# Performance work log

Hardware: AMD Instinct MI355X
Metric: run time of the kernel (lower is better)

## Reference

```python
import jax, jax.numpy as jnp
import numpy as np

N = 100000
E = 1600000
G = 64  # number of graphs
H = 128
BN_EPS = 1e-5


def setup_inputs() -> dict:
    key = jax.random.key(0)
    ks = jax.random.split(key, 12)
    x = jax.random.normal(ks[0], (N, 3), dtype=jnp.float32)
    edge_index = jax.random.randint(ks[1], (2, E), 0, N, dtype=jnp.int64)
    batch = jnp.sort(jax.random.randint(ks[2], (N,), 0, G, dtype=jnp.int64))
    W1 = jax.random.normal(ks[3], (3, H), dtype=jnp.float32) * 0.3
    W2 = jax.random.normal(ks[4], (H, H), dtype=jnp.float32) * 0.05
    W3 = jax.random.normal(ks[5], (H, H), dtype=jnp.float32) * 0.05
    lin_W = jax.random.normal(ks[6], (H, 2), dtype=jnp.float32) * 0.05
    d = {
        'x': x, 'edge_index': edge_index, 'batch': batch,
        'W1': W1, 'b1': jnp.zeros((H,), jnp.float32),
        'W2': W2, 'b2': jnp.zeros((H,), jnp.float32),
        'W3': W3, 'b3': jnp.zeros((H,), jnp.float32),
        'lin_W': lin_W, 'lin_b': jnp.zeros((2,), jnp.float32),
    }
    for i, kk in zip((1, 2, 3), ks[7:10]):
        d[f'bn{i}_g'] = jnp.ones((H,), jnp.float32)
        d[f'bn{i}_b'] = jnp.zeros((H,), jnp.float32)
        d[f'bn{i}_m'] = jnp.zeros((H,), jnp.float32)
        d[f'bn{i}_v'] = jax.random.uniform(kk, (H,), dtype=jnp.float32, minval=0.5, maxval=1.5)
    return d


def _gcn(x, src, dst, norm, W, b):
    # GCNConv: out = scatter_add(norm * (xW)[src], dst) + b
    h = x @ W
    msg = h[src] * norm[:, None]
    agg = jax.ops.segment_sum(msg, dst, num_segments=N)
    return agg + b


def _bn_eval(x, g, b, m, v):
    return (x - m) * jax.lax.rsqrt(v + BN_EPS) * g + b


def reference(x, edge_index, batch, W1, b1, W2, b2, W3, b3,
              bn1_g, bn1_b, bn1_m, bn1_v,
              bn2_g, bn2_b, bn2_m, bn2_v,
              bn3_g, bn3_b, bn3_m, bn3_v,
              lin_W, lin_b):
    loop = jnp.arange(N, dtype=edge_index.dtype)
    src = jnp.concatenate([edge_index[0], loop])
    dst = jnp.concatenate([edge_index[1], loop])
    # symmetric normalization with self-loops: deg from destination nodes
    deg = jax.ops.segment_sum(jnp.ones_like(dst, dtype=x.dtype), dst, num_segments=N)
    dinv = jnp.where(deg > 0, jax.lax.rsqrt(deg), 0.0)
    norm = dinv[src] * dinv[dst]

    h = jax.nn.relu(_bn_eval(_gcn(x, src, dst, norm, W1, b1), bn1_g, bn1_b, bn1_m, bn1_v))
    h = jax.nn.relu(_bn_eval(_gcn(h, src, dst, norm, W2, b2), bn2_g, bn2_b, bn2_m, bn2_v))
    h = jax.nn.relu(_bn_eval(_gcn(h, src, dst, norm, W3, b3), bn3_g, bn3_b, bn3_m, bn3_v))
    # dropout is identity in eval mode
    sums = jax.ops.segment_sum(h, batch, num_segments=G)
    cnts = jax.ops.segment_sum(jnp.ones((N,), h.dtype), batch, num_segments=G)
    pooled = sums / jnp.maximum(cnts, 1.0)[:, None]
    return pooled @ lin_W + lin_b
```

## Files before the change

kernel.cpp:

```cpp
#include <hip/hip_runtime.h>

#define NN 100000
#define EE 1600000
#define GG 64
#define HH 128
#define BN_EPS 1e-5f

#define CB 782
#define NB 256
#define TILE 6250

typedef unsigned short ushort_t;

static __device__ inline ushort_t f2bf(float f) {
    unsigned u = __float_as_uint(f);
    unsigned r = (u + 0x7FFF + ((u >> 16) & 1)) >> 16;
    return (ushort_t)r;
}
static __device__ inline float bf2f(ushort_t b) {
    return __uint_as_float(((unsigned)b) << 16);
}


__global__ __launch_bounds__(256) void k_hist(const int* __restrict__ ei,
                                              int* __restrict__ histG) {
    __shared__ int h[CB];
    int t = threadIdx.x;
    for (int i = t; i < CB; i += 256) h[i] = 0;
    __syncthreads();
    int e0 = blockIdx.x * TILE;
    for (int i = t; i < TILE; i += 256) {
        int d = ei[EE + e0 + i];
        atomicAdd(&h[d >> 7], 1);
    }
    __syncthreads();
    for (int i = t; i < CB; i += 256) histG[blockIdx.x * CB + i] = h[i];
}

__global__ __launch_bounds__(NB) void k_bscan(int* __restrict__ histG,
                                              int* __restrict__ total) {
    __shared__ int sh[NB];
    int t = threadIdx.x;
    int c = blockIdx.x;
    sh[t] = histG[t * CB + c];
    __syncthreads();
    for (int d = 1; d < NB; d <<= 1) {
        int x = (t >= d) ? sh[t - d] : 0;
        __syncthreads();
        sh[t] += x;
        __syncthreads();
    }
    histG[t * CB + c] = (t > 0) ? sh[t - 1] : 0;
    if (t == NB - 1) total[c] = sh[NB - 1];
}

__global__ __launch_bounds__(1024) void k_cbase(const int* __restrict__ total,
                                                int* __restrict__ cbase) {
    __shared__ int sh[1024];
    int t = threadIdx.x;
    sh[t] = (t < CB) ? total[t] : 0;
    __syncthreads();
    for (int d = 1; d < 1024; d <<= 1) {
        int x = (t >= d) ? sh[t - d] : 0;
        __syncthreads();
        sh[t] += x;
        __syncthreads();
    }
    if (t < CB) cbase[t] = (t > 0) ? sh[t - 1] : 0;
    if (t == CB - 1) cbase[CB] = sh[t];
}

__global__ __launch_bounds__(256) void k_cscatter(const int* __restrict__ ei,
                                                  const int* __restrict__ histG,
                                                  const int* __restrict__ cbase,
                                                  int* __restrict__ metaS) {
    __shared__ int base_l[CB];
    __shared__ int cur_l[CB];
    int t = threadIdx.x;
    int b = blockIdx.x;
    for (int i = t; i < CB; i += 256) {
        base_l[i] = cbase[i] + histG[b * CB + i];
        cur_l[i] = 0;
    }
    __syncthreads();
    int e0 = b * TILE;
    for (int i = t; i < TILE; i += 256) {
        int s = ei[e0 + i];
        int d = ei[EE + e0 + i];
        int c = d >> 7;
        int p = base_l[c] + atomicAdd(&cur_l[c], 1);
        metaS[p] = s | ((d & 127) << 17);
    }
}

__global__ __launch_bounds__(256) void k_fine(const int* __restrict__ metaS,
                                              const int* __restrict__ cbase,
                                              int* __restrict__ cnt,
                                              int* __restrict__ offs,
                                              int* __restrict__ col,
                                              float* __restrict__ dinv) {
    __shared__ int hist[128];
    __shared__ int scn[128];
    __shared__ int cur[128];
    int t = threadIdx.x;
    int c = blockIdx.x;
    int lo = cbase[c], hi = cbase[c + 1];
    if (t < 128) hist[t] = 0;
    __syncthreads();
    for (int r = lo + t; r < hi; r += 256) atomicAdd(&hist[metaS[r] >> 17], 1);
    __syncthreads();
    if (t < 128) scn[t] = hist[t];
    __syncthreads();
    for (int d = 1; d < 128; d <<= 1) {
        int x = (t >= d && t < 128) ? scn[t - d] : 0;
        __syncthreads();
        if (t < 128) scn[t] += x;
        __syncthreads();
    }
    if (t < 128) {
        int excl = (t > 0) ? scn[t - 1] : 0;
        cur[t] = excl;
        int node = c * 128 + t;
        if (node < NN) {
            cnt[node] = hist[t];
            offs[node] = lo + excl;
            dinv[node] = rsqrtf((float)(hist[t] + 1));
        }
    }
    __syncthreads();
    for (int r = lo + t; r < hi; r += 256) {
        int pk = metaS[r];
        int s = pk & 0x1FFFF;
        int idx = atomicAdd(&cur[pk >> 17], 1);
        col[lo + idx] = s;
    }
}


__global__ __launch_bounds__(256) void k_l12(const float* __restrict__ x,
                                             const int* __restrict__ offs,
                                             const int* __restrict__ cnt,
                                             const int* __restrict__ col,
                                             const float* __restrict__ dinv,
                                             const float* __restrict__ W1,
                                             const float* __restrict__ b1,
                                             const float* __restrict__ g1,
                                             const float* __restrict__ bb1,
                                             const float* __restrict__ m1,
                                             const float* __restrict__ v1,
                                             const float* __restrict__ W2,
                                             ushort_t* __restrict__ outB) {
    __shared__ float xs[64][132];
    __shared__ float4 ag[64];
    int tid = threadIdx.x;
    int row0 = blockIdx.x * 64;
    int hw = tid >> 5;
    int l = tid & 31;
    for (int k = 0; k < 8; k++) {
        int r = hw * 8 + k;
        int d = row0 + r;
        float a0 = 0.f, a1 = 0.f, a2 = 0.f;
        if (d < NN) {
            float dv = dinv[d];
            int base = offs[d], cn2 = cnt[d];
            for (int i = l; i < cn2; i += 32) {
                int s = col[base + i];
                float w = dinv[s] * dv;
                a0 += w * x[s * 3 + 0];
                a1 += w * x[s * 3 + 1];
                a2 += w * x[s * 3 + 2];
            }
#pragma unroll
            for (int off = 16; off >= 1; off >>= 1) {
                a0 += __shfl_xor(a0, off, 32);
                a1 += __shfl_xor(a1, off, 32);
                a2 += __shfl_xor(a2, off, 32);
            }
            if (l == 0) {
                float w0 = dv * dv;
                a0 += w0 * x[d * 3 + 0];
                a1 += w0 * x[d * 3 + 1];
                a2 += w0 * x[d * 3 + 2];
                ag[r] = make_float4(a0, a1, a2, 0.f);
            }
        } else if (l == 0) {
            ag[r] = make_float4(0.f, 0.f, 0.f, 0.f);
        }
    }
    __syncthreads();
    {
        int c = tid & 127;
        int rh = tid >> 7;
        float w0 = W1[c], w1 = W1[128 + c], w2 = W1[256 + c];
        float sc = g1[c] * rsqrtf(v1[c] + BN_EPS);
        float sh = (b1[c] - m1[c]) * sc + bb1[c];
#pragma unroll
        for (int i = 0; i < 32; i++) {
            int r = 2 * i + rh;
            float4 a = ag[r];
            float t = a.x * w0 + a.y * w1 + a.z * w2;
            xs[r][c] = fmaxf(t * sc + sh, 0.f);
        }
    }
    __syncthreads();
    int tx = tid & 31;
    int ty = tid >> 5;
    float acc[8][4];
#pragma unroll
    for (int i = 0; i < 8; i++)
#pragma unroll
        for (int j = 0; j < 4; j++) acc[i][j] = 0.f;
    const float* Wp = W2 + tx * 4;
#pragma unroll 4
    for (int k = 0; k < 128; k++) {
        float4 w = *(const float4*)&Wp[k * HH];
#pragma unroll
        for (int i = 0; i < 8; i++) {
            float xv = xs[ty * 8 + i][k];
            acc[i][0] += xv * w.x;
            acc[i][1] += xv * w.y;
            acc[i][2] += xv * w.z;
            acc[i][3] += xv * w.w;
        }
    }
    int c0 = tx * 4;
#pragma unroll
    for (int i = 0; i < 8; i++) {
        int gr = row0 + ty * 8 + i;
        if (gr < NN) {
            ushort4 o;
            o.x = f2bf(acc[i][0]);
            o.y = f2bf(acc[i][1]);
            o.z = f2bf(acc[i][2]);
            o.w = f2bf(acc[i][3]);
            size_t addr = (size_t)(c0 >> 6) * NN * 64 + (size_t)gr * 64 + (c0 & 63);
            *(ushort4*)&outB[addr] = o;
        }
    }
}


__global__ __launch_bounds__(256) void k_agg2(const ushort_t* __restrict__ t,
                                              const int* __restrict__ offs,
                                              const int* __restrict__ cnt,
                                              const int* __restrict__ col,
                                              const float* __restrict__ dinv,
                                              const float* __restrict__ bias,
                                              const float* __restrict__ g,
                                              const float* __restrict__ bb,
                                              const float* __restrict__ m,
                                              const float* __restrict__ v,
                                              ushort_t* __restrict__ out) {
    int slice = blockIdx.x & 1;
    int chunk = blockIdx.x >> 1;
    int tid = threadIdx.x;
    int lane = tid & 63;
    int wave = tid >> 6;
    int grp = lane >> 4;
    int l = lane & 15;
    int r = wave * 4 + grp;
    int d = chunk * 16 + r;
    int cl = l * 4;
    int c = slice * 64 + cl;
    const ushort_t* tS = t + (size_t)slice * NN * 64;
    float dvd = dinv[d];
    float w00 = dvd * dvd;
    ushort4 selfR = *(const ushort4*)&tS[(size_t)d * 64 + cl];
    float4 acc;
    acc.x = bf2f(selfR.x) * w00; acc.y = bf2f(selfR.y) * w00;
    acc.z = bf2f(selfR.z) * w00; acc.w = bf2f(selfR.w) * w00;
    int base = offs[d], cn2 = cnt[d];
    int lb = lane & ~15;
    for (int ib = 0; ib < cn2; ib += 16) {
        int i = ib + l;
        int s = 0;
        float w = 0.f;
        if (i < cn2) {
            s = col[base + i];
            w = dinv[s] * dvd;
        }
        int lim = min(16, cn2 - ib);
#pragma unroll 4
        for (int j = 0; j < lim; j++) {
            int ss = __shfl(s, lb + j);
            float ww = __shfl(w, lb + j);
            ushort4 tv = *(const ushort4*)&tS[(size_t)ss * 64 + cl];
            acc.x += ww * bf2f(tv.x);
            acc.y += ww * bf2f(tv.y);
            acc.z += ww * bf2f(tv.z);
            acc.w += ww * bf2f(tv.w);
        }
    }
    float4 gg = *(const float4*)&g[c];
    float4 vv = *(const float4*)&v[c];
    float4 mm = *(const float4*)&m[c];
    float4 bv = *(const float4*)&bb[c];
    float4 bi = *(const float4*)&bias[c];
    float sc0 = gg.x * rsqrtf(vv.x + BN_EPS);
    float sc1 = gg.y * rsqrtf(vv.y + BN_EPS);
    float sc2 = gg.z * rsqrtf(vv.z + BN_EPS);
    float sc3 = gg.w * rsqrtf(vv.w + BN_EPS);
    ushort4 o;
    o.x = f2bf(fmaxf(acc.x * sc0 + (bi.x - mm.x) * sc0 + bv.x, 0.f));
    o.y = f2bf(fmaxf(acc.y * sc1 + (bi.y - mm.y) * sc1 + bv.y, 0.f));
    o.z = f2bf(fmaxf(acc.z * sc2 + (bi.z - mm.z) * sc2 + bv.z, 0.f));
    o.w = f2bf(fmaxf(acc.w * sc3 + (bi.w - mm.w) * sc3 + bv.w, 0.f));
    *(ushort4*)&out[(size_t)slice * NN * 64 + (size_t)d * 64 + cl] = o;
}


__global__ __launch_bounds__(256) void k_mm(const ushort_t* __restrict__ xin,
                                            const float* __restrict__ W,
                                            ushort_t* __restrict__ outB) {
    __shared__ float xs[64][132];
    int tid = threadIdx.x;
    int tx = tid & 31;
    int ty = tid >> 5;
    int row0 = blockIdx.x * 64;
#pragma unroll
    for (int i = 0; i < 4; i++) {
        int idx8 = i * 256 + tid;
        int r = idx8 >> 4;
        int k8 = (idx8 & 15) * 8;
        int gr = row0 + r;
        size_t addr = (size_t)(k8 >> 6) * NN * 64 + (size_t)gr * 64 + (k8 & 63);
        int4 pk = (gr < NN) ? *(const int4*)&xin[addr] : make_int4(0, 0, 0, 0);
        float* dst = &xs[r][k8];
        dst[0] = __uint_as_float(((unsigned)pk.x) << 16);
        dst[1] = __uint_as_float(((unsigned)pk.x) & 0xFFFF0000u);
        dst[2] = __uint_as_float(((unsigned)pk.y) << 16);
        dst[3] = __uint_as_float(((unsigned)pk.y) & 0xFFFF0000u);
        dst[4] = __uint_as_float(((unsigned)pk.z) << 16);
        dst[5] = __uint_as_float(((unsigned)pk.z) & 0xFFFF0000u);
        dst[6] = __uint_as_float(((unsigned)pk.w) << 16);
        dst[7] = __uint_as_float(((unsigned)pk.w) & 0xFFFF0000u);
    }
    __syncthreads();
    float acc[8][4];
#pragma unroll
    for (int i = 0; i < 8; i++)
#pragma unroll
        for (int j = 0; j < 4; j++) acc[i][j] = 0.f;

    const float* Wp = W + tx * 4;
#pragma unroll 4
    for (int k = 0; k < 128; k++) {
        float4 w = *(const float4*)&Wp[k * HH];
#pragma unroll
        for (int i = 0; i < 8; i++) {
            float xv = xs[ty * 8 + i][k];
            acc[i][0] += xv * w.x;
            acc[i][1] += xv * w.y;
            acc[i][2] += xv * w.z;
            acc[i][3] += xv * w.w;
        }
    }
    int c0 = tx * 4;
#pragma unroll
    for (int i = 0; i < 8; i++) {
        int gr = row0 + ty * 8 + i;
        if (gr < NN) {
            ushort4 o;
            o.x = f2bf(acc[i][0]);
            o.y = f2bf(acc[i][1]);
            o.z = f2bf(acc[i][2]);
            o.w = f2bf(acc[i][3]);
            size_t addr = (size_t)(c0 >> 6) * NN * 64 + (size_t)gr * 64 + (c0 & 63);
            *(ushort4*)&outB[addr] = o;
        }
    }
}


__global__ __launch_bounds__(256) void k_aggpool2(const ushort_t* __restrict__ t,
                                                  const int* __restrict__ offs,
                                                  const int* __restrict__ cnt,
                                                  const int* __restrict__ col,
                                                  const float* __restrict__ dinv,
                                                  const float* __restrict__ bias,
                                                  const float* __restrict__ g,
                                                  const float* __restrict__ bb,
                                                  const float* __restrict__ m,
                                                  const float* __restrict__ v,
                                                  const int* __restrict__ batch,
                                                  float* __restrict__ gsum,
                                                  int* __restrict__ gcnt) {
    __shared__ float sh[16][64];
    __shared__ int bsh[16];
    int slice = blockIdx.x & 1;
    int chunk = blockIdx.x >> 1;
    int tid = threadIdx.x;
    int lane = tid & 63;
    int wave = tid >> 6;
    int grp = lane >> 4;
    int l = lane & 15;
    int r = wave * 4 + grp;
    int d = chunk * 16 + r;
    int cl = l * 4;
    int c = slice * 64 + cl;
    if (tid < 16) bsh[tid] = batch[chunk * 16 + tid];
    const ushort_t* tS = t + (size_t)slice * NN * 64;
    float dvd = dinv[d];
    float w00 = dvd * dvd;
    ushort4 selfR = *(const ushort4*)&tS[(size_t)d * 64 + cl];
    float4 acc;
    acc.x = bf2f(selfR.x) * w00; acc.y = bf2f(selfR.y) * w00;
    acc.z = bf2f(selfR.z) * w00; acc.w = bf2f(selfR.w) * w00;
    int base = offs[d], cn2 = cnt[d];
    int lb = lane & ~15;
    for (int ib = 0; ib < cn2; ib += 16) {
        int i = ib + l;
        int s = 0;
        float w = 0.f;
        if (i < cn2) {
            s = col[base + i];
            w = dinv[s] * dvd;
        }
        int lim = min(16, cn2 - ib);
#pragma unroll 4
        for (int j = 0; j < lim; j++) {
            int ss = __shfl(s, lb + j);
            float ww = __shfl(w, lb + j);
            ushort4 tv = *(const ushort4*)&tS[(size_t)ss * 64 + cl];
            acc.x += ww * bf2f(tv.x);
            acc.y += ww * bf2f(tv.y);
            acc.z += ww * bf2f(tv.z);
            acc.w += ww * bf2f(tv.w);
        }
    }
    float4 gg = *(const float4*)&g[c];
    float4 vv = *(const float4*)&v[c];
    float4 mm = *(const float4*)&m[c];
    float4 bv = *(const float4*)&bb[c];
    float4 bi = *(const float4*)&bias[c];
    float sc0 = gg.x * rsqrtf(vv.x + BN_EPS);
    float sc1 = gg.y * rsqrtf(vv.y + BN_EPS);
    float sc2 = gg.z * rsqrtf(vv.z + BN_EPS);
    float sc3 = gg.w * rsqrtf(vv.w + BN_EPS);
    float4 o;
    o.x = fmaxf(acc.x * sc0 + (bi.x - mm.x) * sc0 + bv.x, 0.f);
    o.y = fmaxf(acc.y * sc1 + (bi.y - mm.y) * sc1 + bv.y, 0.f);
    o.z = fmaxf(acc.z * sc2 + (bi.z - mm.z) * sc2 + bv.z, 0.f);
    o.w = fmaxf(acc.w * sc3 + (bi.w - mm.w) * sc3 + bv.w, 0.f);
    *(float4*)&sh[r][cl] = o;
    __syncthreads();
    if (tid < 64) {
        int cc = tid;
        float acc2 = 0.f;
        int cur = bsh[0];
        for (int rr = 0; rr < 16; rr++) {
            int g2 = bsh[rr];
            if (g2 != cur) {
                atomicAdd(&gsum[cur * HH + slice * 64 + cc], acc2);
                acc2 = 0.f; cur = g2;
            }
            acc2 += sh[rr][cc];
        }
        atomicAdd(&gsum[cur * HH + slice * 64 + cc], acc2);
    } else if (tid == 64 && slice == 0) {
        int cur = bsh[0];
        int count = 0;
        for (int rr = 0; rr < 16; rr++) {
            int g2 = bsh[rr];
            if (g2 != cur) {
                atomicAdd(&gcnt[cur], count);
                count = 0; cur = g2;
            }
            count++;
        }
        atomicAdd(&gcnt[cur], count);
    }
}

__global__ void k_head(const float* __restrict__ gsum, const int* __restrict__ gcnt,
                       const float* __restrict__ linW, const float* __restrict__ linb,
                       float* __restrict__ out) {
    int t = threadIdx.x;
    int gr = t >> 1, j = t & 1;
    float inv = 1.0f / fmaxf((float)gcnt[gr], 1.0f);
    float acc = 0.f;
    for (int c = 0; c < HH; c++) acc += gsum[gr * HH + c] * linW[c * 2 + j];
    out[t] = acc * inv + linb[j];
}


static inline size_t al256(size_t x) { return (x + 255) & ~(size_t)255; }

extern "C" void kernel_launch(void* const* d_in, const int* in_sizes, int n_in,
                              void* d_out, int out_size, void* d_ws, size_t ws_size,
                              hipStream_t stream) {
    const float* x    = (const float*)d_in[0];
    const int*   ei   = (const int*)d_in[1];
    const int*   batch= (const int*)d_in[2];
    const float* W1   = (const float*)d_in[3];
    const float* b1   = (const float*)d_in[4];
    const float* W2   = (const float*)d_in[5];
    const float* b2   = (const float*)d_in[6];
    const float* W3   = (const float*)d_in[7];
    const float* b3   = (const float*)d_in[8];
    const float* linW = (const float*)d_in[9];
    const float* linb = (const float*)d_in[10];
    const float* bn1g = (const float*)d_in[11];
    const float* bn1b = (const float*)d_in[12];
    const float* bn1m = (const float*)d_in[13];
    const float* bn1v = (const float*)d_in[14];
    const float* bn2g = (const float*)d_in[15];
    const float* bn2b = (const float*)d_in[16];
    const float* bn2m = (const float*)d_in[17];
    const float* bn2v = (const float*)d_in[18];
    const float* bn3g = (const float*)d_in[19];
    const float* bn3b = (const float*)d_in[20];
    const float* bn3m = (const float*)d_in[21];
    const float* bn3v = (const float*)d_in[22];
    float* out = (float*)d_out;

    char* ws = (char*)d_ws;
    size_t off = 0;
    int*    histG  = (int*)(ws + off);    off += al256((size_t)NB * CB * 4);
    int*    total  = (int*)(ws + off);    off += al256((size_t)CB * 4);
    int*    cbase  = (int*)(ws + off);    off += al256((size_t)(CB + 1) * 4);
    int*    cnt    = (int*)(ws + off);    off += al256((size_t)NN * 4);
    int*    offs   = (int*)(ws + off);    off += al256((size_t)NN * 4);
    float*  dinv   = (float*)(ws + off);  off += al256((size_t)NN * 4);
    int*    col    = (int*)(ws + off);    off += al256((size_t)(EE + 64) * 4);
    char*   buf2   = (char*)(ws + off);   off += al256((size_t)NN * HH * 2);
    char*   buf3   = (char*)(ws + off);   off += al256((size_t)NN * HH * 2);
    float*  gsum   = (float*)(ws + off);  off += (size_t)GG * HH * 4;
    int*    gcnt   = (int*)(ws + off);    off += al256((size_t)GG * 4);

    int* metaS = (int*)buf2;
    ushort_t* t2 = (ushort_t*)buf2;
    ushort_t* h2 = (ushort_t*)buf3;

    hipMemsetAsync(gsum, 0, (size_t)GG * HH * 4 + (size_t)GG * 4, stream);

    k_hist<<<NB, 256, 0, stream>>>(ei, histG);
    k_bscan<<<CB, NB, 0, stream>>>(histG, total);
    k_cbase<<<1, 1024, 0, stream>>>(total, cbase);
    k_cscatter<<<NB, 256, 0, stream>>>(ei, histG, cbase, metaS);
    k_fine<<<CB, 256, 0, stream>>>(metaS, cbase, cnt, offs, col, dinv);

    int nblk64 = (NN + 63) / 64;
    int nblkS  = (NN / 16) * 2;

    k_l12<<<nblk64, 256, 0, stream>>>(x, offs, cnt, col, dinv,
                                      W1, b1, bn1g, bn1b, bn1m, bn1v, W2, t2);

    k_agg2<<<nblkS, 256, 0, stream>>>(t2, offs, cnt, col, dinv,
                                      b2, bn2g, bn2b, bn2m, bn2v, h2);

    k_mm<<<nblk64, 256, 0, stream>>>(h2, W3, t2);

    k_aggpool2<<<nblkS, 256, 0, stream>>>(t2, offs, cnt, col, dinv,
                                          b3, bn3g, bn3b, bn3m, bn3v,
                                          batch, gsum, gcnt);

    k_head<<<1, 128, 0, stream>>>(gsum, gcnt, linW, linb, out);
}
```

Before: 461.7 us.

## Use row-major bf16 features and precomputed edge weights in aggregation

Replaces the two-slice (64-column split) feature layout with a plain row-major 128-column bf16 layout. Each aggregation now processes a full 256-byte row per 32-lane half-wave, so every neighbour gather is one contiguous row read and col/weight metadata is read once rather than once per slice. Per-edge normalisation weights are computed and stored in the first layer, which removes the dinv[s] random gather in later layers. The cost is an extra 6.4MB weight array that is written and then read twice, and twice as many ushort4 loads in flight per neighbour row.

```diff
diff --git a/kernel.cpp b/kernel.cpp
--- a/kernel.cpp
+++ b/kernel.cpp
@@ -142,6 +142,7 @@
                                              const int* __restrict__ cnt,
                                              const int* __restrict__ col,
                                              const float* __restrict__ dinv,
+                                             float* __restrict__ wgt,
                                              const float* __restrict__ W1,
                                              const float* __restrict__ b1,
                                              const float* __restrict__ g1,
@@ -166,6 +167,7 @@
             for (int i = l; i < cn2; i += 32) {
                 int s = col[base + i];
                 float w = dinv[s] * dv;
+                wgt[base + i] = w;
                 a0 += w * x[s * 3 + 0];
                 a1 += w * x[s * 3 + 1];
                 a2 += w * x[s * 3 + 2];
@@ -223,7 +225,6 @@
             acc[i][3] += xv * w.w;
         }
     }
-    int c0 = tx * 4;
 #pragma unroll
     for (int i = 0; i < 8; i++) {
         int gr = row0 + ty * 8 + i;
@@ -233,69 +234,62 @@
             o.y = f2bf(acc[i][1]);
             o.z = f2bf(acc[i][2]);
             o.w = f2bf(acc[i][3]);
-            size_t addr = (size_t)(c0 >> 6) * NN * 64 + (size_t)gr * 64 + (c0 & 63);
-            *(ushort4*)&outB[addr] = o;
-        }
-    }
-}
-
-
-__global__ __launch_bounds__(256) void k_agg2(const ushort_t* __restrict__ t,
-                                              const int* __restrict__ offs,
-                                              const int* __restrict__ cnt,
-                                              const int* __restrict__ col,
-                                              const float* __restrict__ dinv,
-                                              const float* __restrict__ bias,
-                                              const float* __restrict__ g,
-                                              const float* __restrict__ bb,
-                                              const float* __restrict__ m,
-                                              const float* __restrict__ v,
-                                              ushort_t* __restrict__ out) {
-    int slice = blockIdx.x & 1;
-    int chunk = blockIdx.x >> 1;
-    int tid = threadIdx.x;
-    int lane = tid & 63;
-    int wave = tid >> 6;
-    int grp = lane >> 4;
-    int l = lane & 15;
-    int r = wave * 4 + grp;
-    int d = chunk * 16 + r;
-    int cl = l * 4;
-    int c = slice * 64 + cl;
-    const ushort_t* tS = t + (size_t)slice * NN * 64;
-    float dvd = dinv[d];
-    float w00 = dvd * dvd;
-    ushort4 selfR = *(const ushort4*)&tS[(size_t)d * 64 + cl];
+            *(ushort4*)&outB[(size_t)gr * HH + tx * 4] = o;
+        }
+    }
+}
+
+
+__global__ __launch_bounds__(256) void k_agg(const ushort_t* __restrict__ t,
+                                             const int* __restrict__ offs,
+                                             const int* __restrict__ cnt,
+                                             const int* __restrict__ col,
+                                             const float* __restrict__ wgt,
+                                             const float* __restrict__ dinv,
+                                             const float* __restrict__ bias,
+                                             const float* __restrict__ g,
+                                             const float* __restrict__ bb,
+                                             const float* __restrict__ m,
+                                             const float* __restrict__ v,
+                                             ushort_t* __restrict__ out) {
+    int wave = threadIdx.x >> 6;
+    int lane = threadIdx.x & 63;
+    int half = lane >> 5;
+    int l = lane & 31;
+    int d = blockIdx.x * 8 + wave * 2 + half;
+    int c0 = l * 4;
+    float dv = dinv[d];
+    float w0 = dv * dv;
+    ushort4 selfR = *(const ushort4*)&t[(size_t)d * HH + c0];
     float4 acc;
-    acc.x = bf2f(selfR.x) * w00; acc.y = bf2f(selfR.y) * w00;
-    acc.z = bf2f(selfR.z) * w00; acc.w = bf2f(selfR.w) * w00;
-    int base = offs[d], cn2 = cnt[d];
-    int lb = lane & ~15;
-    for (int ib = 0; ib < cn2; ib += 16) {
+    acc.x = bf2f(selfR.x) * w0; acc.y = bf2f(selfR.y) * w0;
+    acc.z = bf2f(selfR.z) * w0; acc.w = bf2f(selfR.w) * w0;
+    int base = offs[d], cn = cnt[d];
+    for (int ib = 0; ib < cn; ib += 32) {
         int i = ib + l;
         int s = 0;
         float w = 0.f;
-        if (i < cn2) {
+        if (i < cn) {
             s = col[base + i];
-            w = dinv[s] * dvd;
-        }
-        int lim = min(16, cn2 - ib);
-#pragma unroll 4
+            w = wgt[base + i];
+        }
+        int lim = min(32, cn - ib);
+#pragma unroll 8
         for (int j = 0; j < lim; j++) {
-            int ss = __shfl(s, lb + j);
-            float ww = __shfl(w, lb + j);
-            ushort4 tv = *(const ushort4*)&tS[(size_t)ss * 64 + cl];
+            int ss = __shfl(s, j, 32);
+            float ww = __shfl(w, j, 32);
+            ushort4 tv = *(const ushort4*)&t[(size_t)ss * HH + c0];
             acc.x += ww * bf2f(tv.x);
             acc.y += ww * bf2f(tv.y);
             acc.z += ww * bf2f(tv.z);
             acc.w += ww * bf2f(tv.w);
         }
     }
-    float4 gg = *(const float4*)&g[c];
-    float4 vv = *(const float4*)&v[c];
-    float4 mm = *(const float4*)&m[c];
-    float4 bv = *(const float4*)&bb[c];
-    float4 bi = *(const float4*)&bias[c];
+    float4 gg = *(const float4*)&g[c0];
+    float4 vv = *(const float4*)&v[c0];
+    float4 mm = *(const float4*)&m[c0];
+    float4 bv = *(const float4*)&bb[c0];
+    float4 bi = *(const float4*)&bias[c0];
     float sc0 = gg.x * rsqrtf(vv.x + BN_EPS);
     float sc1 = gg.y * rsqrtf(vv.y + BN_EPS);
     float sc2 = gg.z * rsqrtf(vv.z + BN_EPS);
@@ -305,7 +299,7 @@
     o.y = f2bf(fmaxf(acc.y * sc1 + (bi.y - mm.y) * sc1 + bv.y, 0.f));
     o.z = f2bf(fmaxf(acc.z * sc2 + (bi.z - mm.z) * sc2 + bv.z, 0.f));
     o.w = f2bf(fmaxf(acc.w * sc3 + (bi.w - mm.w) * sc3 + bv.w, 0.f));
-    *(ushort4*)&out[(size_t)slice * NN * 64 + (size_t)d * 64 + cl] = o;
+    *(ushort4*)&out[(size_t)d * HH + c0] = o;
 }
 
 
@@ -323,8 +317,8 @@
         int r = idx8 >> 4;
         int k8 = (idx8 & 15) * 8;
         int gr = row0 + r;
-        size_t addr = (size_t)(k8 >> 6) * NN * 64 + (size_t)gr * 64 + (k8 & 63);
-        int4 pk = (gr < NN) ? *(const int4*)&xin[addr] : make_int4(0, 0, 0, 0);
+        int4 pk = (gr < NN) ? *(const int4*)&xin[(size_t)gr * HH + k8]
+                            : make_int4(0, 0, 0, 0);
         float* dst = &xs[r][k8];
         dst[0] = __uint_as_float(((unsigned)pk.x) << 16);
         dst[1] = __uint_as_float(((unsigned)pk.x) & 0xFFFF0000u);
@@ -355,7 +349,6 @@
             acc[i][3] += xv * w.w;
         }
     }
-    int c0 = tx * 4;
 #pragma unroll
     for (int i = 0; i < 8; i++) {
         int gr = row0 + ty * 8 + i;
@@ -365,74 +358,68 @@
             o.y = f2bf(acc[i][1]);
             o.z = f2bf(acc[i][2]);
             o.w = f2bf(acc[i][3]);
-            size_t addr = (size_t)(c0 >> 6) * NN * 64 + (size_t)gr * 64 + (c0 & 63);
-            *(ushort4*)&outB[addr] = o;
-        }
-    }
-}
-
-
-__global__ __launch_bounds__(256) void k_aggpool2(const ushort_t* __restrict__ t,
-                                                  const int* __restrict__ offs,
-                                                  const int* __restrict__ cnt,
-                                                  const int* __restrict__ col,
-                                                  const float* __restrict__ dinv,
-                                                  const float* __restrict__ bias,
-                                                  const float* __restrict__ g,
-                                                  const float* __restrict__ bb,
-                                                  const float* __restrict__ m,
-                                                  const float* __restrict__ v,
-                                                  const int* __restrict__ batch,
-                                                  float* __restrict__ gsum,
-                                                  int* __restrict__ gcnt) {
-    __shared__ float sh[16][64];
-    __shared__ int bsh[16];
-    int slice = blockIdx.x & 1;
-    int chunk = blockIdx.x >> 1;
-    int tid = threadIdx.x;
-    int lane = tid & 63;
-    int wave = tid >> 6;
-    int grp = lane >> 4;
-    int l = lane & 15;
-    int r = wave * 4 + grp;
-    int d = chunk * 16 + r;
-    int cl = l * 4;
-    int c = slice * 64 + cl;
-    if (tid < 16) bsh[tid] = batch[chunk * 16 + tid];
-    const ushort_t* tS = t + (size_t)slice * NN * 64;
-    float dvd = dinv[d];
-    float w00 = dvd * dvd;
-    ushort4 selfR = *(const ushort4*)&tS[(size_t)d * 64 + cl];
+            *(ushort4*)&outB[(size_t)gr * HH + tx * 4] = o;
+        }
+    }
+}
+
+
+__global__ __launch_bounds__(256) void k_aggpool(const ushort_t* __restrict__ t,
+                                                 const int* __restrict__ offs,
+                                                 const int* __restrict__ cnt,
+                                                 const int* __restrict__ col,
+                                                 const float* __restrict__ wgt,
+                                                 const float* __restrict__ dinv,
+                                                 const float* __restrict__ bias,
+                                                 const float* __restrict__ g,
+                                                 const float* __restrict__ bb,
+                                                 const float* __restrict__ m,
+                                                 const float* __restrict__ v,
+                                                 const int* __restrict__ batch,
+                                                 float* __restrict__ gsum,
+                                                 int* __restrict__ gcnt) {
+    __shared__ float sh[8][128];
+    __shared__ int bsh[8];
+    int wave = threadIdx.x >> 6;
+    int lane = threadIdx.x & 63;
+    int half = lane >> 5;
+    int l = lane & 31;
+    int r = wave * 2 + half;
+    int d = blockIdx.x * 8 + r;
+    int c0 = l * 4;
+    if (threadIdx.x < 8) bsh[threadIdx.x] = batch[blockIdx.x * 8 + threadIdx.x];
+    float dv = dinv[d];
+    float w0 = dv * dv;
+    ushort4 selfR = *(const ushort4*)&t[(size_t)d * HH + c0];
     float4 acc;
-    acc.x = bf2f(selfR.x) * w00; acc.y = bf2f(selfR.y) * w00;
-    acc.z = bf2f(selfR.z) * w00; acc.w = bf2f(selfR.w) * w00;
-    int base = offs[d], cn2 = cnt[d];
-    int lb = lane & ~15;
-    for (int ib = 0; ib < cn2; ib += 16) {
+    acc.x = bf2f(selfR.x) * w0; acc.y = bf2f(selfR.y) * w0;
+    acc.z = bf2f(selfR.z) * w0; acc.w = bf2f(selfR.w) * w0;
+    int base = offs[d], cn = cnt[d];
+    for (int ib = 0; ib < cn; ib += 32) {
         int i = ib + l;
         int s = 0;
         float w = 0.f;
-        if (i < cn2) {
+        if (i < cn) {
             s = col[base + i];
-            w = dinv[s] * dvd;
-        }
-        int lim = min(16, cn2 - ib);
-#pragma unroll 4
+            w = wgt[base + i];
+        }
+        int lim = min(32, cn - ib);
+#pragma unroll 8
         for (int j = 0; j < lim; j++) {
-            int ss = __shfl(s, lb + j);
-            float ww = __shfl(w, lb + j);
-            ushort4 tv = *(const ushort4*)&tS[(size_t)ss * 64 + cl];
+            int ss = __shfl(s, j, 32);
+            float ww = __shfl(w, j, 32);
+            ushort4 tv = *(const ushort4*)&t[(size_t)ss * HH + c0];
             acc.x += ww * bf2f(tv.x);
             acc.y += ww * bf2f(tv.y);
             acc.z += ww * bf2f(tv.z);
             acc.w += ww * bf2f(tv.w);
         }
     }
-    float4 gg = *(const float4*)&g[c];
-    float4 vv = *(const float4*)&v[c];
-    float4 mm = *(const float4*)&m[c];
-    float4 bv = *(const float4*)&bb[c];
-    float4 bi = *(const float4*)&bias[c];
+    float4 gg = *(const float4*)&g[c0];
+    float4 vv = *(const float4*)&v[c0];
+    float4 mm = *(const float4*)&m[c0];
+    float4 bv = *(const float4*)&bb[c0];
+    float4 bi = *(const float4*)&bias[c0];
     float sc0 = gg.x * rsqrtf(vv.x + BN_EPS);
     float sc1 = gg.y * rsqrtf(vv.y + BN_EPS);
     float sc2 = gg.z * rsqrtf(vv.z + BN_EPS);
@@ -442,25 +429,27 @@
     o.y = fmaxf(acc.y * sc1 + (bi.y - mm.y) * sc1 + bv.y, 0.f);
     o.z = fmaxf(acc.z * sc2 + (bi.z - mm.z) * sc2 + bv.z, 0.f);
     o.w = fmaxf(acc.w * sc3 + (bi.w - mm.w) * sc3 + bv.w, 0.f);
-    *(float4*)&sh[r][cl] = o;
-    __syncthreads();
-    if (tid < 64) {
-        int cc = tid;
-        float acc2 = 0.f;
+    *(float4*)&sh[r][c0] = o;
+    __syncthreads();
+    if (threadIdx.x < 128) {
+        int c = threadIdx.x;
+        float a = 0.f;
         int cur = bsh[0];
-        for (int rr = 0; rr < 16; rr++) {
+#pragma unroll
+        for (int rr = 0; rr < 8; rr++) {
             int g2 = bsh[rr];
             if (g2 != cur) {
-                atomicAdd(&gsum[cur * HH + slice * 64 + cc], acc2);
-                acc2 = 0.f; cur = g2;
+                atomicAdd(&gsum[cur * HH + c], a);
+                a = 0.f; cur = g2;
             }
-            acc2 += sh[rr][cc];
-        }
-        atomicAdd(&gsum[cur * HH + slice * 64 + cc], acc2);
-    } else if (tid == 64 && slice == 0) {
+            a += sh[rr][c];
+        }
+        atomicAdd(&gsum[cur * HH + c], a);
+    } else if (threadIdx.x == 128) {
         int cur = bsh[0];
         int count = 0;
-        for (int rr = 0; rr < 16; rr++) {
+#pragma unroll
+        for (int rr = 0; rr < 8; rr++) {
             int g2 = bsh[rr];
             if (g2 != cur) {
                 atomicAdd(&gcnt[cur], count);
@@ -523,6 +512,7 @@
     int*    offs   = (int*)(ws + off);    off += al256((size_t)NN * 4);
     float*  dinv   = (float*)(ws + off);  off += al256((size_t)NN * 4);
     int*    col    = (int*)(ws + off);    off += al256((size_t)(EE + 64) * 4);
+    float*  wgt    = (float*)(ws + off);  off += al256((size_t)(EE + 64) * 4);
     char*   buf2   = (char*)(ws + off);   off += al256((size_t)NN * HH * 2);
     char*   buf3   = (char*)(ws + off);   off += al256((size_t)NN * HH * 2);
     float*  gsum   = (float*)(ws + off);  off += (size_t)GG * HH * 4;
@@ -541,17 +531,16 @@
     k_fine<<<CB, 256, 0, stream>>>(metaS, cbase, cnt, offs, col, dinv);
 
     int nblk64 = (NN + 63) / 64;
-    int nblkS  = (NN / 16) * 2;
-
-    k_l12<<<nblk64, 256, 0, stream>>>(x, offs, cnt, col, dinv,
+
+    k_l12<<<nblk64, 256, 0, stream>>>(x, offs, cnt, col, dinv, wgt,
                                       W1, b1, bn1g, bn1b, bn1m, bn1v, W2, t2);
 
-    k_agg2<<<nblkS, 256, 0, stream>>>(t2, offs, cnt, col, dinv,
+    k_agg<<<NN / 8, 256, 0, stream>>>(t2, offs, cnt, col, wgt, dinv,
                                       b2, bn2g, bn2b, bn2m, bn2v, h2);
 
     k_mm<<<nblk64, 256, 0, stream>>>(h2, W3, t2);
 
-    k_aggpool2<<<nblkS, 256, 0, stream>>>(t2, offs, cnt, col, dinv,
+    k_aggpool<<<NN / 8, 256, 0, stream>>>(t2, offs, cnt, col, wgt, dinv,
                                           b3, bn3g, bn3b, bn3m, bn3v,
                                           batch, gsum, gcnt);
 
```

Result: no change. 468.3 us (+1.4%).
